# Kernel optimization log

Hardware: AMD Instinct MI355X
Metric: run time of the kernel (lower is better)

## Reference

```python
import jax, jax.numpy as jnp
import numpy as np

L = 5          # num_layer
D = 128        # emb_dim
F = 16         # raw node/edge feature dim
N = 50000      # nodes
E = 800000     # edges
BN_EPS = 1e-5


def _bn(z, g, b):
    # BatchNorm1d forward with batch statistics (training-mode math)
    m = z.mean(axis=0)
    v = z.var(axis=0)
    return (z - m) * jax.lax.rsqrt(v + BN_EPS) * g + b


def setup_inputs() -> dict:
    key = jax.random.key(0)
    ks = jax.random.split(key, 8)
    s = lambda *sh: 0.05  # weight scale
    return {
        "x": jax.random.normal(ks[0], (N, F), jnp.float32),
        "edge_index": jax.random.randint(ks[1], (2, E), 0, N, jnp.int32),
        "edge_attr": jax.random.normal(ks[2], (E, F), jnp.float32),
        "W_node": jax.random.normal(ks[3], (F, D), jnp.float32) * 0.05,
        "b_node": jnp.zeros((D,), jnp.float32),
        "We": jax.random.normal(ks[4], (L, F, D), jnp.float32) * 0.05,
        "be": jnp.zeros((L, D), jnp.float32),
        "eps_gin": jnp.zeros((L,), jnp.float32),
        "W1": jax.random.normal(ks[5], (L, D, 2 * D), jnp.float32) * 0.05,
        "b1": jnp.zeros((L, 2 * D), jnp.float32),
        "g1": jnp.ones((L, 2 * D), jnp.float32),
        "beta1": jnp.zeros((L, 2 * D), jnp.float32),
        "W2": jax.random.normal(ks[6], (L, 2 * D, D), jnp.float32) * 0.05,
        "b2": jnp.zeros((L, D), jnp.float32),
        "g_bn": jnp.ones((L, D), jnp.float32),
        "beta_bn": jnp.zeros((L, D), jnp.float32),
    }


def reference(x, edge_index, edge_attr, W_node, b_node, We, be, eps_gin,
              W1, b1, g1, beta1, W2, b2, g_bn, beta_bn):
    src, dst = edge_index[0], edge_index[1]
    n = x.shape[0]
    h = x @ W_node + b_node                       # node encoder: [N, D]
    for l in range(L):
        e = edge_attr @ We[l] + be[l]             # edge encoder: [E, D]
        msg = jax.nn.relu(h[src] + e)             # gather + message
        agg = jax.ops.segment_sum(msg, dst, num_segments=n)  # scatter-add
        z = (1.0 + eps_gin[l]) * h + agg
        z = _bn(z @ W1[l] + b1[l], g1[l], beta1[l])  # GIN MLP hidden
        z = jax.nn.relu(z)
        z = z @ W2[l] + b2[l]                     # GIN MLP out: [N, D]
        z = _bn(z, g_bn[l], beta_bn[l])           # per-layer BatchNorm
        if l < L - 1:
            z = jax.nn.relu(z)                    # dropout is identity (p=0)
        h = z + h                                 # residual
    return h                                      # JK = 'last'
```

## Files before the change

kernel.cpp:

```cpp
#include <hip/hip_runtime.h>
#include <hip/hip_bf16.h>

#define NN 50000
#define EE 800000
#define DD 128
#define FF 16
#define LL 5
#define NPART 3125

typedef __attribute__((ext_vector_type(8))) short bf16x8;
typedef __attribute__((ext_vector_type(4))) float f32x4;

__device__ __forceinline__ unsigned short f2bf(float f) {
    union { float f; unsigned int u; } v; v.f = f;
    unsigned int u = v.u;
    unsigned int r = (u + 0x7fffu + ((u >> 16) & 1u)) >> 16;
    return (unsigned short)r;
}
__device__ __forceinline__ float bf2f(unsigned short s) {
    union { unsigned int u; float f; } v; v.u = ((unsigned int)s) << 16;
    return v.f;
}
#define BFLO(u) __uint_as_float((unsigned int)(u) << 16)
#define BFHI(u) __uint_as_float((unsigned int)(u) & 0xffff0000u)

__global__ void k_node_enc(const float* __restrict__ x, const float* __restrict__ Wn,
                           const float* __restrict__ bn, float* __restrict__ h,
                           unsigned short* __restrict__ h_bf)
{
    const int t = blockIdx.x * 256 + threadIdx.x;
    const int i = t >> 7, d = t & 127;
    const float4* x4 = (const float4*)(x + (size_t)i * 16);
    float4 a0 = x4[0], a1 = x4[1], a2 = x4[2], a3 = x4[3];
    float acc = bn[d];
    acc += a0.x*Wn[0*128+d] + a0.y*Wn[1*128+d] + a0.z*Wn[2*128+d] + a0.w*Wn[3*128+d];
    acc += a1.x*Wn[4*128+d] + a1.y*Wn[5*128+d] + a1.z*Wn[6*128+d] + a1.w*Wn[7*128+d];
    acc += a2.x*Wn[8*128+d] + a2.y*Wn[9*128+d] + a2.z*Wn[10*128+d] + a2.w*Wn[11*128+d];
    acc += a3.x*Wn[12*128+d] + a3.y*Wn[13*128+d] + a3.z*Wn[14*128+d] + a3.w*Wn[15*128+d];
    h[t] = acc;
    h_bf[t] = f2bf(acc);
}

__global__ void k_count(const int* __restrict__ ei, int* __restrict__ counts)
{
    const int e = blockIdx.x * 256 + threadIdx.x;
    atomicAdd(&counts[ei[EE + e]], 1);
}

__global__ __launch_bounds__(1024) void k_scan(int* __restrict__ counts, int* __restrict__ row_ptr)
{
    __shared__ int wsum[16];
    __shared__ int carry;
    const int tid = threadIdx.x, lane = tid & 63, w = tid >> 6;
    if (tid == 0) carry = 0;
    __syncthreads();
    for (int base = 0; base < NN; base += 1024) {
        const int i = base + tid;
        const int v = (i < NN) ? counts[i] : 0;
        int x = v;
        #pragma unroll
        for (int off = 1; off < 64; off <<= 1) {
            const int t = __shfl_up(x, off);
            if (lane >= off) x += t;
        }
        if (lane == 63) wsum[w] = x;
        __syncthreads();
        int woff = 0, total = 0;
        #pragma unroll
        for (int j = 0; j < 16; ++j) { const int s = wsum[j]; total += s; if (j < w) woff += s; }
        const int ex = carry + woff + x - v;
        if (i < NN) { row_ptr[i] = ex; counts[i] = ex; }
        __syncthreads();
        if (tid == 0) carry += total;
        __syncthreads();
    }
    if (tid == 0) row_ptr[NN] = carry;
}

__global__ void k_fill(const int* __restrict__ ei, const float* __restrict__ ea,
                       int* __restrict__ cursor, int* __restrict__ src_perm,
                       unsigned short* __restrict__ ea_bf)
{
    const int e = blockIdx.x * 256 + threadIdx.x;
    const int dst = ei[EE + e];
    const int p = atomicAdd(&cursor[dst], 1);
    src_perm[p] = ei[e];
    const float4* s4 = (const float4*)(ea + (size_t)e * 16);
    const float4 a0 = s4[0], a1 = s4[1], a2 = s4[2], a3 = s4[3];
    union { bf16x8 v; unsigned short u[8]; } o0, o1;
    o0.u[0]=f2bf(a0.x); o0.u[1]=f2bf(a0.y); o0.u[2]=f2bf(a0.z); o0.u[3]=f2bf(a0.w);
    o0.u[4]=f2bf(a1.x); o0.u[5]=f2bf(a1.y); o0.u[6]=f2bf(a1.z); o0.u[7]=f2bf(a1.w);
    o1.u[0]=f2bf(a2.x); o1.u[1]=f2bf(a2.y); o1.u[2]=f2bf(a2.z); o1.u[3]=f2bf(a2.w);
    o1.u[4]=f2bf(a3.x); o1.u[5]=f2bf(a3.y); o1.u[6]=f2bf(a3.z); o1.u[7]=f2bf(a3.w);
    bf16x8* dp = (bf16x8*)(ea_bf + (size_t)p * 16);
    dp[0] = o0.v; dp[1] = o1.v;
}

__global__ void k_pack(const float* __restrict__ W1, const float* __restrict__ W2,
                       unsigned short* __restrict__ Wp1, unsigned short* __restrict__ Wp2)
{
    int t = blockIdx.x * 256 + threadIdx.x;
    const int total = LL * 32768;
    if (t < total) {
        const int l = t >> 15, r = t & 32767;
        const int j = r & 7, lane = (r >> 3) & 63, kt = (r >> 9) & 3, nt = r >> 11;
        const int k = kt * 32 + (lane >> 4) * 8 + j;
        const int n = nt * 16 + (lane & 15);
        Wp1[t] = f2bf(W1[(size_t)l * 32768 + k * 256 + n]);
    } else {
        t -= total;
        const int l = t >> 15, r = t & 32767;
        const int j = r & 7, lane = (r >> 3) & 63, kt = (r >> 9) & 7, nt = r >> 12;
        const int k = kt * 32 + (lane >> 4) * 8 + j;
        const int n = nt * 16 + (lane & 15);
        Wp2[t] = f2bf(W2[(size_t)l * 32768 + k * 128 + n]);
    }
}

__global__ __launch_bounds__(256) void k_agg(
    const unsigned short* __restrict__ h_bf, const unsigned short* __restrict__ ea_bf,
    const float* __restrict__ We_l, const float* __restrict__ be_l,
    const float* __restrict__ eps_gin, const int l,
    const int* __restrict__ row_ptr, const int* __restrict__ src_perm,
    unsigned short* __restrict__ z_bf)
{
    const int wv = threadIdx.x >> 6;
    const int v  = blockIdx.x * 4 + wv;
    const int lane = threadIdx.x & 63;
    const int c2 = lane * 2;
    float2 w[16];
    #pragma unroll
    for (int f = 0; f < 16; ++f) w[f] = *(const float2*)(We_l + f * 128 + c2);
    const float2 bed = *(const float2*)(be_l + c2);
    const float epsv = 1.0f + eps_gin[l];
    const int kbeg = __builtin_amdgcn_readfirstlane(row_ptr[v]);
    const int kend = __builtin_amdgcn_readfirstlane(row_ptr[v + 1]);
    float2 acc0 = {0.f,0.f}, acc1 = {0.f,0.f}, acc2 = {0.f,0.f}, acc3 = {0.f,0.f};

#define LOAD_GROUP(kk, S0,S1,S2,S3, E0,E1,E2,E3,E4,E5,E6,E7, H0,H1,H2,H3)  \
    { const int* sp_ = src_perm + (kk);                                     \
      S0 = __builtin_amdgcn_readfirstlane(sp_[0]);                          \
      S1 = __builtin_amdgcn_readfirstlane(sp_[1]);                          \
      S2 = __builtin_amdgcn_readfirstlane(sp_[2]);                          \
      S3 = __builtin_amdgcn_readfirstlane(sp_[3]);                          \
      const uint4* ep_ = (const uint4*)(ea_bf + (size_t)(kk) * 16);         \
      E0 = ep_[0]; E1 = ep_[1]; E2 = ep_[2]; E3 = ep_[3];                   \
      E4 = ep_[4]; E5 = ep_[5]; E6 = ep_[6]; E7 = ep_[7];                   \
      H0 = *(const unsigned int*)(h_bf + (size_t)S0 * 128 + c2);            \
      H1 = *(const unsigned int*)(h_bf + (size_t)S1 * 128 + c2);            \
      H2 = *(const unsigned int*)(h_bf + (size_t)S2 * 128 + c2);            \
      H3 = *(const unsigned int*)(h_bf + (size_t)S3 * 128 + c2); }

#define EDGE_DOT(EA, EB, HQ, OUT) do {                                      \
        float ex_ = bed.x, ey_ = bed.y, a_;                                 \
        a_ = BFLO(EA.x); ex_ += a_*w[0].x;  ey_ += a_*w[0].y;               \
        a_ = BFHI(EA.x); ex_ += a_*w[1].x;  ey_ += a_*w[1].y;               \
        a_ = BFLO(EA.y); ex_ += a_*w[2].x;  ey_ += a_*w[2].y;               \
        a_ = BFHI(EA.y); ex_ += a_*w[3].x;  ey_ += a_*w[3].y;               \
        a_ = BFLO(EA.z); ex_ += a_*w[4].x;  ey_ += a_*w[4].y;               \
        a_ = BFHI(EA.z); ex_ += a_*w[5].x;  ey_ += a_*w[5].y;               \
        a_ = BFLO(EA.w); ex_ += a_*w[6].x;  ey_ += a_*w[6].y;               \
        a_ = BFHI(EA.w); ex_ += a_*w[7].x;  ey_ += a_*w[7].y;               \
        a_ = BFLO(EB.x); ex_ += a_*w[8].x;  ey_ += a_*w[8].y;               \
        a_ = BFHI(EB.x); ex_ += a_*w[9].x;  ey_ += a_*w[9].y;               \
        a_ = BFLO(EB.y); ex_ += a_*w[10].x; ey_ += a_*w[10].y;              \
        a_ = BFHI(EB.y); ex_ += a_*w[11].x; ey_ += a_*w[11].y;              \
        a_ = BFLO(EB.z); ex_ += a_*w[12].x; ey_ += a_*w[12].y;              \
        a_ = BFHI(EB.z); ex_ += a_*w[13].x; ey_ += a_*w[13].y;              \
        a_ = BFLO(EB.w); ex_ += a_*w[14].x; ey_ += a_*w[14].y;              \
        a_ = BFHI(EB.w); ex_ += a_*w[15].x; ey_ += a_*w[15].y;              \
        const float mx_ = BFLO(HQ) + ex_, my_ = BFHI(HQ) + ey_;             \
        OUT.x += mx_ > 0.f ? mx_ : 0.f;                                     \
        OUT.y += my_ > 0.f ? my_ : 0.f;                                     \
    } while (0)

    int k = kbeg;
    int cs0, cs1, cs2, cs3;
    uint4 ce0, ce1, ce2, ce3, ce4, ce5, ce6, ce7;
    unsigned int ch0, ch1, ch2, ch3;
    if (k < kend) {
        LOAD_GROUP(k, cs0,cs1,cs2,cs3, ce0,ce1,ce2,ce3,ce4,ce5,ce6,ce7, ch0,ch1,ch2,ch3);
    }
    for (; k < kend; k += 4) {
        int ns0, ns1, ns2, ns3;
        uint4 ne0, ne1, ne2, ne3, ne4, ne5, ne6, ne7;
        unsigned int nh0, nh1, nh2, nh3;
        LOAD_GROUP(k + 4, ns0,ns1,ns2,ns3, ne0,ne1,ne2,ne3,ne4,ne5,ne6,ne7, nh0,nh1,nh2,nh3);
        EDGE_DOT(ce0, ce1, ch0, acc0);
        if (k + 1 < kend) EDGE_DOT(ce2, ce3, ch1, acc1);
        if (k + 2 < kend) EDGE_DOT(ce4, ce5, ch2, acc2);
        if (k + 3 < kend) EDGE_DOT(ce6, ce7, ch3, acc3);
        cs0=ns0; cs1=ns1; cs2=ns2; cs3=ns3;
        ce0=ne0; ce1=ne1; ce2=ne2; ce3=ne3; ce4=ne4; ce5=ne5; ce6=ne6; ce7=ne7;
        ch0=nh0; ch1=nh1; ch2=nh2; ch3=nh3;
    }
#undef EDGE_DOT
#undef LOAD_GROUP
    (void)cs0; (void)cs1; (void)cs2; (void)cs3;
    const unsigned int hv = *(const unsigned int*)(h_bf + (size_t)v * 128 + c2);
    const float zx = epsv * BFLO(hv) + ((acc0.x + acc1.x) + (acc2.x + acc3.x));
    const float zy = epsv * BFHI(hv) + ((acc0.y + acc1.y) + (acc2.y + acc3.y));
    const unsigned int zp = (unsigned int)f2bf(zx) | ((unsigned int)f2bf(zy) << 16);
    *(unsigned int*)(z_bf + (size_t)v * 128 + c2) = zp;
}

__global__ __launch_bounds__(256) void k_gemmB(
    const unsigned short* __restrict__ z_bf,
    const unsigned short* __restrict__ Wp,
    unsigned short* __restrict__ t_bf,
    float* __restrict__ ps, float* __restrict__ pq)
{
    __shared__ __align__(16) unsigned short zs[16 * 136];
    const int tid = threadIdx.x;
    const int r0 = blockIdx.x * 16;
    {
        const int row = tid & 15, c0 = (tid >> 4) * 8;
        *(bf16x8*)(&zs[row * 136 + c0]) =
            *(const bf16x8*)(z_bf + (size_t)(r0 + row) * 128 + c0);
    }
    __syncthreads();
    const int w = tid >> 6, l6 = tid & 63, m = l6 & 15, quad = l6 >> 4;
    const f32x4 z4 = {0.f, 0.f, 0.f, 0.f};
    f32x4 acc[4] = {z4, z4, z4, z4};
    const bf16x8* Wv = (const bf16x8*)Wp;
    #pragma unroll
    for (int kt = 0; kt < 4; ++kt) {
        const bf16x8 a = *(const bf16x8*)(&zs[m * 136 + kt * 32 + quad * 8]);
        #pragma unroll
        for (int f = 0; f < 4; ++f) {
            const bf16x8 b = Wv[((w * 4 + f) * 4 + kt) * 64 + l6];
            acc[f] = __builtin_amdgcn_mfma_f32_16x16x32_bf16(a, b, acc[f], 0, 0, 0);
        }
    }
    const int rowb = r0 + quad * 4;
    #pragma unroll
    for (int f = 0; f < 4; ++f) {
        const int col = w * 64 + f * 16 + m;
        float ssum = 0.f, ssq = 0.f;
        #pragma unroll
        for (int r = 0; r < 4; ++r) {
            const float val = acc[f][r];
            t_bf[(size_t)(rowb + r) * 256 + col] = f2bf(val);
            ssum += val; ssq += val * val;
        }
        ssum += __shfl_xor(ssum, 16); ssum += __shfl_xor(ssum, 32);
        ssq  += __shfl_xor(ssq , 16); ssq  += __shfl_xor(ssq , 32);
        if (quad == 0) {
            ps[(size_t)col * NPART + blockIdx.x] = ssum;
            pq[(size_t)col * NPART + blockIdx.x] = ssq;
        }
    }
}

__global__ void k_bnstat(const float* __restrict__ ps, const float* __restrict__ pq,
                         const float* __restrict__ g, const float* __restrict__ beta,
                         float* __restrict__ sc, float* __restrict__ sh)
{
    const int c = blockIdx.x;
    const int tid = threadIdx.x;
    const float* pr = ps + (size_t)c * NPART;
    const float* qr = pq + (size_t)c * NPART;
    float s = 0.f, q = 0.f;
    for (int i = tid; i < NPART; i += 256) { s += pr[i]; q += qr[i]; }
    #pragma unroll
    for (int off = 1; off < 64; off <<= 1) { s += __shfl_xor(s, off); q += __shfl_xor(q, off); }
    __shared__ float ls[4], lq[4];
    const int wv = tid >> 6;
    if ((tid & 63) == 0) { ls[wv] = s; lq[wv] = q; }
    __syncthreads();
    if (tid == 0) {
        const float S = ls[0] + ls[1] + ls[2] + ls[3];
        const float Q = lq[0] + lq[1] + lq[2] + lq[3];
        const float mean = S * (1.0f / NN);
        const float var  = Q * (1.0f / NN) - mean * mean;
        const float rs = rsqrtf(var + 1e-5f);
        const float scale = g[c] * rs;
        sc[c] = scale;
        sh[c] = beta[c] - mean * scale;
    }
}

__global__ __launch_bounds__(128) void k_gemmD(
    const unsigned short* __restrict__ t_bf,
    const float* __restrict__ sc1, const float* __restrict__ sh1,
    const unsigned short* __restrict__ Wp,
    unsigned short* __restrict__ vb,
    float* __restrict__ ps, float* __restrict__ pq)
{
    __shared__ __align__(16) unsigned short us[16 * 264];
    const int tid = threadIdx.x;
    const int r0 = blockIdx.x * 16;
    {
        const int row = tid & 15, g8 = (tid >> 4) * 8;
        #pragma unroll
        for (int cc = 0; cc < 4; ++cc) {
            const int c = cc * 64 + g8;
            union { bf16x8 v; unsigned short u[8]; } in, o;
            in.v = *(const bf16x8*)(t_bf + (size_t)(r0 + row) * 256 + c);
            const float4* scp = (const float4*)(sc1 + c);
            const float4* shp = (const float4*)(sh1 + c);
            const float4 s0 = scp[0], s1 = scp[1], b0 = shp[0], b1 = shp[1];
            float xv;
            xv = bf2f(in.u[0])*s0.x + b0.x; o.u[0] = f2bf(xv > 0.f ? xv : 0.f);
            xv = bf2f(in.u[1])*s0.y + b0.y; o.u[1] = f2bf(xv > 0.f ? xv : 0.f);
            xv = bf2f(in.u[2])*s0.z + b0.z; o.u[2] = f2bf(xv > 0.f ? xv : 0.f);
            xv = bf2f(in.u[3])*s0.w + b0.w; o.u[3] = f2bf(xv > 0.f ? xv : 0.f);
            xv = bf2f(in.u[4])*s1.x + b1.x; o.u[4] = f2bf(xv > 0.f ? xv : 0.f);
            xv = bf2f(in.u[5])*s1.y + b1.y; o.u[5] = f2bf(xv > 0.f ? xv : 0.f);
            xv = bf2f(in.u[6])*s1.z + b1.z; o.u[6] = f2bf(xv > 0.f ? xv : 0.f);
            xv = bf2f(in.u[7])*s1.w + b1.w; o.u[7] = f2bf(xv > 0.f ? xv : 0.f);
            *(bf16x8*)(&us[row * 264 + c]) = o.v;
        }
    }
    __syncthreads();
    const int w = tid >> 6, l6 = tid & 63, m = l6 & 15, quad = l6 >> 4;
    const f32x4 z4 = {0.f, 0.f, 0.f, 0.f};
    f32x4 acc[4] = {z4, z4, z4, z4};
    const bf16x8* Wv = (const bf16x8*)Wp;
    #pragma unroll
    for (int kt = 0; kt < 8; ++kt) {
        const bf16x8 a = *(const bf16x8*)(&us[m * 264 + kt * 32 + quad * 8]);
        #pragma unroll
        for (int f = 0; f < 4; ++f) {
            const bf16x8 b = Wv[((w * 4 + f) * 8 + kt) * 64 + l6];
            acc[f] = __builtin_amdgcn_mfma_f32_16x16x32_bf16(a, b, acc[f], 0, 0, 0);
        }
    }
    const int rowb = r0 + quad * 4;
    #pragma unroll
    for (int f = 0; f < 4; ++f) {
        const int col = w * 64 + f * 16 + m;
        float ssum = 0.f, ssq = 0.f;
        #pragma unroll
        for (int r = 0; r < 4; ++r) {
            const float val = acc[f][r];
            vb[(size_t)(rowb + r) * 128 + col] = f2bf(val);
            ssum += val; ssq += val * val;
        }
        ssum += __shfl_xor(ssum, 16); ssum += __shfl_xor(ssum, 32);
        ssq  += __shfl_xor(ssq , 16); ssq  += __shfl_xor(ssq , 32);
        if (quad == 0) {
            ps[(size_t)col * NPART + blockIdx.x] = ssum;
            pq[(size_t)col * NPART + blockIdx.x] = ssq;
        }
    }
}

__global__ void k_fin(const unsigned short* __restrict__ vb,
                      const float* __restrict__ sc2, const float* __restrict__ sh2,
                      float* __restrict__ h, unsigned short* __restrict__ h_bf,
                      const int do_relu)
{
    const int t = blockIdx.x * 256 + threadIdx.x;
    const int base = t * 8;
    const int c = base & 127;
    union { bf16x8 v; unsigned short u[8]; } in, ob;
    in.v = *(const bf16x8*)(vb + base);
    const float4 s0 = *(const float4*)(sc2 + c), s1 = *(const float4*)(sc2 + c + 4);
    const float4 b0 = *(const float4*)(sh2 + c), b1 = *(const float4*)(sh2 + c + 4);
    float4 h0 = *(const float4*)(h + base), h1 = *(const float4*)(h + base + 4);
    float z;
    z = bf2f(in.u[0])*s0.x + b0.x; if (do_relu) z = z > 0.f ? z : 0.f; h0.x += z;
    z = bf2f(in.u[1])*s0.y + b0.y; if (do_relu) z = z > 0.f ? z : 0.f; h0.y += z;
    z = bf2f(in.u[2])*s0.z + b0.z; if (do_relu) z = z > 0.f ? z : 0.f; h0.z += z;
    z = bf2f(in.u[3])*s0.w + b0.w; if (do_relu) z = z > 0.f ? z : 0.f; h0.w += z;
    z = bf2f(in.u[4])*s1.x + b1.x; if (do_relu) z = z > 0.f ? z : 0.f; h1.x += z;
    z = bf2f(in.u[5])*s1.y + b1.y; if (do_relu) z = z > 0.f ? z : 0.f; h1.y += z;
    z = bf2f(in.u[6])*s1.z + b1.z; if (do_relu) z = z > 0.f ? z : 0.f; h1.z += z;
    z = bf2f(in.u[7])*s1.w + b1.w; if (do_relu) z = z > 0.f ? z : 0.f; h1.w += z;
    *(float4*)(h + base) = h0;
    *(float4*)(h + base + 4) = h1;
    ob.u[0]=f2bf(h0.x); ob.u[1]=f2bf(h0.y); ob.u[2]=f2bf(h0.z); ob.u[3]=f2bf(h0.w);
    ob.u[4]=f2bf(h1.x); ob.u[5]=f2bf(h1.y); ob.u[6]=f2bf(h1.z); ob.u[7]=f2bf(h1.w);
    *(bf16x8*)(h_bf + base) = ob.v;
}

extern "C" void kernel_launch(void* const* d_in, const int* in_sizes, int n_in,
                              void* d_out, int out_size, void* d_ws, size_t ws_size,
                              hipStream_t stream)
{
    const float* x       = (const float*)d_in[0];
    const int*   ei      = (const int*)  d_in[1];
    const float* ea      = (const float*)d_in[2];
    const float* W_node  = (const float*)d_in[3];
    const float* b_node  = (const float*)d_in[4];
    const float* We      = (const float*)d_in[5];
    const float* be      = (const float*)d_in[6];
    const float* eps_gin = (const float*)d_in[7];
    const float* W1      = (const float*)d_in[8];
    const float* g1      = (const float*)d_in[10];
    const float* beta1   = (const float*)d_in[11];
    const float* W2      = (const float*)d_in[12];
    const float* g_bn    = (const float*)d_in[14];
    const float* beta_bn = (const float*)d_in[15];

    float* h = (float*)d_out;

    char* W = (char*)d_ws;
    int*   counts   = (int*)  (W + 0);
    int*   row_ptr  = (int*)  (W + 200000);
    float* sc1      = (float*)(W + 400016);
    float* sh1      = (float*)(W + 401040);
    float* sc2      = (float*)(W + 402064);
    float* sh2      = (float*)(W + 402576);
    float* ps1      = (float*)(W + 403088);
    float* pq1      = (float*)(W + 3603088);
    float* ps2      = (float*)(W + 6803088);
    float* pq2      = (float*)(W + 8403088);
    int*   src_perm = (int*)  (W + 10003088);
    unsigned short* ea_bf = (unsigned short*)(W + 13203120);
    unsigned short* Wp1   = (unsigned short*)(W + 38803376);
    unsigned short* Wp2   = (unsigned short*)(W + 39131056);
    unsigned short* z_bf  = (unsigned short*)(W + 39458736);
    unsigned short* t_bf  = (unsigned short*)(W + 52258736);
    unsigned short* h_bf  = (unsigned short*)(W + 77858736);
    unsigned short* vb    = z_bf;

    (void)hipMemsetAsync(counts, 0, 200000, stream);
    (void)hipMemsetAsync(src_perm + EE, 0, 32, stream);

    k_node_enc<<<dim3(NN * DD / 256), dim3(256), 0, stream>>>(x, W_node, b_node, h, h_bf);
    k_count<<<dim3(EE / 256), dim3(256), 0, stream>>>(ei, counts);
    k_scan<<<dim3(1), dim3(1024), 0, stream>>>(counts, row_ptr);
    k_fill<<<dim3(EE / 256), dim3(256), 0, stream>>>(ei, ea, counts, src_perm, ea_bf);
    k_pack<<<dim3(2 * LL * 32768 / 256), dim3(256), 0, stream>>>(W1, W2, Wp1, Wp2);

    for (int l = 0; l < LL; ++l) {
        k_agg<<<dim3(NN / 4), dim3(256), 0, stream>>>(
            h_bf, ea_bf, We + (size_t)l * FF * DD, be + (size_t)l * DD,
            eps_gin, l, row_ptr, src_perm, z_bf);
        k_gemmB<<<dim3(NPART), dim3(256), 0, stream>>>(
            z_bf, Wp1 + (size_t)l * 32768, t_bf, ps1, pq1);
        k_bnstat<<<dim3(256), dim3(256), 0, stream>>>(
            ps1, pq1, g1 + (size_t)l * 256, beta1 + (size_t)l * 256, sc1, sh1);
        k_gemmD<<<dim3(NPART), dim3(128), 0, stream>>>(
            t_bf, sc1, sh1, Wp2 + (size_t)l * 32768, vb, ps2, pq2);
        k_bnstat<<<dim3(128), dim3(256), 0, stream>>>(
            ps2, pq2, g_bn + (size_t)l * 128, beta_bn + (size_t)l * 128, sc2, sh2);
        k_fin<<<dim3(NN * DD / 8 / 256), dim3(256), 0, stream>>>(
            vb, sc2, sh2, h, h_bf, (l < LL - 1) ? 1 : 0);
    }
}
```

Measured before the change: 949.9 us.

## Retile GIN GEMMs to 64-row blocks and deepen index prefetch in aggregation

The two MLP GEMM kernels now process 64 rows per block, with each wave computing a 16-row strip across all output columns. This cuts the block count and raises the MFMA work done per block, with guarded tail rows and per-wave partial statistics. The aggregation kernel prefetches source indices two groups ahead and adds a scheduling barrier so gather latency overlaps compute. The tradeoffs are higher register pressure, fewer blocks to fill the GPU, and extra padding in the index buffer.

Result: slower. 1.051 ms (+10.7%).

```diff
diff --git a/kernel.cpp b/kernel.cpp
--- a/kernel.cpp
+++ b/kernel.cpp
@@ -6,7 +6,8 @@
 #define DD 128
 #define FF 16
 #define LL 5
-#define NPART 3125
+#define NB 782
+#define NPART (NB * 4)
 
 typedef __attribute__((ext_vector_type(8))) short bf16x8;
 typedef __attribute__((ext_vector_type(4))) float f32x4;
@@ -136,20 +137,6 @@
     const int kbeg = __builtin_amdgcn_readfirstlane(row_ptr[v]);
     const int kend = __builtin_amdgcn_readfirstlane(row_ptr[v + 1]);
     float2 acc0 = {0.f,0.f}, acc1 = {0.f,0.f}, acc2 = {0.f,0.f}, acc3 = {0.f,0.f};
-
-#define LOAD_GROUP(kk, S0,S1,S2,S3, E0,E1,E2,E3,E4,E5,E6,E7, H0,H1,H2,H3)  \
-    { const int* sp_ = src_perm + (kk);                                     \
-      S0 = __builtin_amdgcn_readfirstlane(sp_[0]);                          \
-      S1 = __builtin_amdgcn_readfirstlane(sp_[1]);                          \
-      S2 = __builtin_amdgcn_readfirstlane(sp_[2]);                          \
-      S3 = __builtin_amdgcn_readfirstlane(sp_[3]);                          \
-      const uint4* ep_ = (const uint4*)(ea_bf + (size_t)(kk) * 16);         \
-      E0 = ep_[0]; E1 = ep_[1]; E2 = ep_[2]; E3 = ep_[3];                   \
-      E4 = ep_[4]; E5 = ep_[5]; E6 = ep_[6]; E7 = ep_[7];                   \
-      H0 = *(const unsigned int*)(h_bf + (size_t)S0 * 128 + c2);            \
-      H1 = *(const unsigned int*)(h_bf + (size_t)S1 * 128 + c2);            \
-      H2 = *(const unsigned int*)(h_bf + (size_t)S2 * 128 + c2);            \
-      H3 = *(const unsigned int*)(h_bf + (size_t)S3 * 128 + c2); }
 
 #define EDGE_DOT(EA, EB, HQ, OUT) do {                                      \
         float ex_ = bed.x, ey_ = bed.y, a_;                                 \
@@ -174,29 +161,50 @@
         OUT.y += my_ > 0.f ? my_ : 0.f;                                     \
     } while (0)
 
-    int k = kbeg;
-    int cs0, cs1, cs2, cs3;
     uint4 ce0, ce1, ce2, ce3, ce4, ce5, ce6, ce7;
     unsigned int ch0, ch1, ch2, ch3;
+    int vs0, vs1, vs2, vs3;
+
+    int k = kbeg;
     if (k < kend) {
-        LOAD_GROUP(k, cs0,cs1,cs2,cs3, ce0,ce1,ce2,ce3,ce4,ce5,ce6,ce7, ch0,ch1,ch2,ch3);
+        const int a0 = __builtin_amdgcn_readfirstlane(src_perm[k]);
+        const int a1 = __builtin_amdgcn_readfirstlane(src_perm[k + 1]);
+        const int a2 = __builtin_amdgcn_readfirstlane(src_perm[k + 2]);
+        const int a3 = __builtin_amdgcn_readfirstlane(src_perm[k + 3]);
+        ch0 = *(const unsigned int*)(h_bf + (size_t)a0 * 128 + c2);
+        ch1 = *(const unsigned int*)(h_bf + (size_t)a1 * 128 + c2);
+        ch2 = *(const unsigned int*)(h_bf + (size_t)a2 * 128 + c2);
+        ch3 = *(const unsigned int*)(h_bf + (size_t)a3 * 128 + c2);
+        const uint4* ep = (const uint4*)(ea_bf + (size_t)k * 16);
+        ce0 = ep[0]; ce1 = ep[1]; ce2 = ep[2]; ce3 = ep[3];
+        ce4 = ep[4]; ce5 = ep[5]; ce6 = ep[6]; ce7 = ep[7];
+        vs0 = src_perm[k + 4]; vs1 = src_perm[k + 5];
+        vs2 = src_perm[k + 6]; vs3 = src_perm[k + 7];
     }
     for (; k < kend; k += 4) {
-        int ns0, ns1, ns2, ns3;
-        uint4 ne0, ne1, ne2, ne3, ne4, ne5, ne6, ne7;
-        unsigned int nh0, nh1, nh2, nh3;
-        LOAD_GROUP(k + 4, ns0,ns1,ns2,ns3, ne0,ne1,ne2,ne3,ne4,ne5,ne6,ne7, nh0,nh1,nh2,nh3);
+        const int fs0 = src_perm[k + 8],  fs1 = src_perm[k + 9];
+        const int fs2 = src_perm[k + 10], fs3 = src_perm[k + 11];
+        const int b0 = __builtin_amdgcn_readfirstlane(vs0);
+        const int b1 = __builtin_amdgcn_readfirstlane(vs1);
+        const int b2 = __builtin_amdgcn_readfirstlane(vs2);
+        const int b3 = __builtin_amdgcn_readfirstlane(vs3);
+        const unsigned int nh0 = *(const unsigned int*)(h_bf + (size_t)b0 * 128 + c2);
+        const unsigned int nh1 = *(const unsigned int*)(h_bf + (size_t)b1 * 128 + c2);
+        const unsigned int nh2 = *(const unsigned int*)(h_bf + (size_t)b2 * 128 + c2);
+        const unsigned int nh3 = *(const unsigned int*)(h_bf + (size_t)b3 * 128 + c2);
+        const uint4* np_ = (const uint4*)(ea_bf + (size_t)(k + 4) * 16);
+        const uint4 ne0 = np_[0], ne1 = np_[1], ne2 = np_[2], ne3 = np_[3];
+        const uint4 ne4 = np_[4], ne5 = np_[5], ne6 = np_[6], ne7 = np_[7];
+        __builtin_amdgcn_sched_barrier(0);
         EDGE_DOT(ce0, ce1, ch0, acc0);
         if (k + 1 < kend) EDGE_DOT(ce2, ce3, ch1, acc1);
         if (k + 2 < kend) EDGE_DOT(ce4, ce5, ch2, acc2);
         if (k + 3 < kend) EDGE_DOT(ce6, ce7, ch3, acc3);
-        cs0=ns0; cs1=ns1; cs2=ns2; cs3=ns3;
         ce0=ne0; ce1=ne1; ce2=ne2; ce3=ne3; ce4=ne4; ce5=ne5; ce6=ne6; ce7=ne7;
         ch0=nh0; ch1=nh1; ch2=nh2; ch3=nh3;
+        vs0=fs0; vs1=fs1; vs2=fs2; vs3=fs3;
     }
 #undef EDGE_DOT
-#undef LOAD_GROUP
-    (void)cs0; (void)cs1; (void)cs2; (void)cs3;
     const unsigned int hv = *(const unsigned int*)(h_bf + (size_t)v * 128 + c2);
     const float zx = epsv * BFLO(hv) + ((acc0.x + acc1.x) + (acc2.x + acc3.x));
     const float zy = epsv * BFHI(hv) + ((acc0.y + acc1.y) + (acc2.y + acc3.y));
@@ -210,44 +218,49 @@
     unsigned short* __restrict__ t_bf,
     float* __restrict__ ps, float* __restrict__ pq)
 {
-    __shared__ __align__(16) unsigned short zs[16 * 136];
+    __shared__ __align__(16) unsigned short zs[64 * 136];
     const int tid = threadIdx.x;
-    const int r0 = blockIdx.x * 16;
+    const int r0 = blockIdx.x * 64;
     {
-        const int row = tid & 15, c0 = (tid >> 4) * 8;
-        *(bf16x8*)(&zs[row * 136 + c0]) =
-            *(const bf16x8*)(z_bf + (size_t)(r0 + row) * 128 + c0);
+        const int rb = tid >> 4, c0 = (tid & 15) * 8;
+        const bf16x8 zero = {0,0,0,0,0,0,0,0};
+        #pragma unroll
+        for (int r = 0; r < 4; ++r) {
+            const int row = r * 16 + rb, g = r0 + row;
+            *(bf16x8*)(&zs[row * 136 + c0]) =
+                (g < NN) ? *(const bf16x8*)(z_bf + (size_t)g * 128 + c0) : zero;
+        }
     }
     __syncthreads();
     const int w = tid >> 6, l6 = tid & 63, m = l6 & 15, quad = l6 >> 4;
     const f32x4 z4 = {0.f, 0.f, 0.f, 0.f};
-    f32x4 acc[4] = {z4, z4, z4, z4};
+    f32x4 acc[16] = {z4,z4,z4,z4,z4,z4,z4,z4,z4,z4,z4,z4,z4,z4,z4,z4};
     const bf16x8* Wv = (const bf16x8*)Wp;
     #pragma unroll
     for (int kt = 0; kt < 4; ++kt) {
-        const bf16x8 a = *(const bf16x8*)(&zs[m * 136 + kt * 32 + quad * 8]);
-        #pragma unroll
-        for (int f = 0; f < 4; ++f) {
-            const bf16x8 b = Wv[((w * 4 + f) * 4 + kt) * 64 + l6];
-            acc[f] = __builtin_amdgcn_mfma_f32_16x16x32_bf16(a, b, acc[f], 0, 0, 0);
-        }
-    }
-    const int rowb = r0 + quad * 4;
-    #pragma unroll
-    for (int f = 0; f < 4; ++f) {
-        const int col = w * 64 + f * 16 + m;
+        const bf16x8 a = *(const bf16x8*)(&zs[(w * 16 + m) * 136 + kt * 32 + quad * 8]);
+        #pragma unroll
+        for (int ct = 0; ct < 16; ++ct) {
+            const bf16x8 b = Wv[(ct * 4 + kt) * 64 + l6];
+            acc[ct] = __builtin_amdgcn_mfma_f32_16x16x32_bf16(a, b, acc[ct], 0, 0, 0);
+        }
+    }
+    const int rowb = r0 + w * 16 + quad * 4;
+    #pragma unroll
+    for (int ct = 0; ct < 16; ++ct) {
+        const int col = ct * 16 + m;
         float ssum = 0.f, ssq = 0.f;
         #pragma unroll
         for (int r = 0; r < 4; ++r) {
-            const float val = acc[f][r];
-            t_bf[(size_t)(rowb + r) * 256 + col] = f2bf(val);
+            const float val = acc[ct][r];
+            if (rowb + r < NN) t_bf[(size_t)(rowb + r) * 256 + col] = f2bf(val);
             ssum += val; ssq += val * val;
         }
         ssum += __shfl_xor(ssum, 16); ssum += __shfl_xor(ssum, 32);
         ssq  += __shfl_xor(ssq , 16); ssq  += __shfl_xor(ssq , 32);
         if (quad == 0) {
-            ps[(size_t)col * NPART + blockIdx.x] = ssum;
-            pq[(size_t)col * NPART + blockIdx.x] = ssq;
+            ps[(size_t)col * NPART + blockIdx.x * 4 + w] = ssum;
+            pq[(size_t)col * NPART + blockIdx.x * 4 + w] = ssq;
         }
     }
 }
@@ -280,68 +293,72 @@
     }
 }
 
-__global__ __launch_bounds__(128) void k_gemmD(
+__global__ __launch_bounds__(256) void k_gemmD(
     const unsigned short* __restrict__ t_bf,
     const float* __restrict__ sc1, const float* __restrict__ sh1,
     const unsigned short* __restrict__ Wp,
     unsigned short* __restrict__ vb,
     float* __restrict__ ps, float* __restrict__ pq)
 {
-    __shared__ __align__(16) unsigned short us[16 * 264];
+    __shared__ __align__(16) unsigned short us[64 * 264];
     const int tid = threadIdx.x;
-    const int r0 = blockIdx.x * 16;
+    const int r0 = blockIdx.x * 64;
     {
-        const int row = tid & 15, g8 = (tid >> 4) * 8;
-        #pragma unroll
-        for (int cc = 0; cc < 4; ++cc) {
-            const int c = cc * 64 + g8;
+        const int rb = tid >> 5, c0 = (tid & 31) * 8;
+        const float4 s0 = *(const float4*)(sc1 + c0), s1 = *(const float4*)(sc1 + c0 + 4);
+        const float4 b0 = *(const float4*)(sh1 + c0), b1 = *(const float4*)(sh1 + c0 + 4);
+        const bf16x8 zero = {0,0,0,0,0,0,0,0};
+        #pragma unroll
+        for (int rr = 0; rr < 8; ++rr) {
+            const int row = rr * 8 + rb, g = r0 + row;
             union { bf16x8 v; unsigned short u[8]; } in, o;
-            in.v = *(const bf16x8*)(t_bf + (size_t)(r0 + row) * 256 + c);
-            const float4* scp = (const float4*)(sc1 + c);
-            const float4* shp = (const float4*)(sh1 + c);
-            const float4 s0 = scp[0], s1 = scp[1], b0 = shp[0], b1 = shp[1];
-            float xv;
-            xv = bf2f(in.u[0])*s0.x + b0.x; o.u[0] = f2bf(xv > 0.f ? xv : 0.f);
-            xv = bf2f(in.u[1])*s0.y + b0.y; o.u[1] = f2bf(xv > 0.f ? xv : 0.f);
-            xv = bf2f(in.u[2])*s0.z + b0.z; o.u[2] = f2bf(xv > 0.f ? xv : 0.f);
-            xv = bf2f(in.u[3])*s0.w + b0.w; o.u[3] = f2bf(xv > 0.f ? xv : 0.f);
-            xv = bf2f(in.u[4])*s1.x + b1.x; o.u[4] = f2bf(xv > 0.f ? xv : 0.f);
-            xv = bf2f(in.u[5])*s1.y + b1.y; o.u[5] = f2bf(xv > 0.f ? xv : 0.f);
-            xv = bf2f(in.u[6])*s1.z + b1.z; o.u[6] = f2bf(xv > 0.f ? xv : 0.f);
-            xv = bf2f(in.u[7])*s1.w + b1.w; o.u[7] = f2bf(xv > 0.f ? xv : 0.f);
-            *(bf16x8*)(&us[row * 264 + c]) = o.v;
+            if (g < NN) {
+                in.v = *(const bf16x8*)(t_bf + (size_t)g * 256 + c0);
+                float xv;
+                xv = bf2f(in.u[0])*s0.x + b0.x; o.u[0] = f2bf(xv > 0.f ? xv : 0.f);
+                xv = bf2f(in.u[1])*s0.y + b0.y; o.u[1] = f2bf(xv > 0.f ? xv : 0.f);
+                xv = bf2f(in.u[2])*s0.z + b0.z; o.u[2] = f2bf(xv > 0.f ? xv : 0.f);
+                xv = bf2f(in.u[3])*s0.w + b0.w; o.u[3] = f2bf(xv > 0.f ? xv : 0.f);
+                xv = bf2f(in.u[4])*s1.x + b1.x; o.u[4] = f2bf(xv > 0.f ? xv : 0.f);
+                xv = bf2f(in.u[5])*s1.y + b1.y; o.u[5] = f2bf(xv > 0.f ? xv : 0.f);
+                xv = bf2f(in.u[6])*s1.z + b1.z; o.u[6] = f2bf(xv > 0.f ? xv : 0.f);
+                xv = bf2f(in.u[7])*s1.w + b1.w; o.u[7] = f2bf(xv > 0.f ? xv : 0.f);
+            } else {
+                o.v = zero;
+            }
+            *(bf16x8*)(&us[row * 264 + c0]) = o.v;
         }
     }
     __syncthreads();
     const int w = tid >> 6, l6 = tid & 63, m = l6 & 15, quad = l6 >> 4;
     const f32x4 z4 = {0.f, 0.f, 0.f, 0.f};
-    f32x4 acc[4] = {z4, z4, z4, z4};
+    f32x4 acc[8] = {z4,z4,z4,z4,z4,z4,z4,z4};
     const bf16x8* Wv = (const bf16x8*)Wp;
     #pragma unroll
     for (int kt = 0; kt < 8; ++kt) {
-        const bf16x8 a = *(const bf16x8*)(&us[m * 264 + kt * 32 + quad * 8]);
-        #pragma unroll
-        for (int f = 0; f < 4; ++f) {
-            const bf16x8 b = Wv[((w * 4 + f) * 8 + kt) * 64 + l6];
-            acc[f] = __builtin_amdgcn_mfma_f32_16x16x32_bf16(a, b, acc[f], 0, 0, 0);
-        }
-    }
-    const int rowb = r0 + quad * 4;
-    #pragma unroll
-    for (int f = 0; f < 4; ++f) {
-        const int col = w * 64 + f * 16 + m;
+        const bf16x8 a = *(const bf16x8*)(&us[(w * 16 + m) * 264 + kt * 32 + quad * 8]);
+        #pragma unroll
+        for (int ct = 0; ct < 8; ++ct) {
+            const bf16x8 b = Wv[(ct * 8 + kt) * 64 + l6];
+            acc[ct] = __builtin_amdgcn_mfma_f32_16x16x32_bf16(a, b, acc[ct], 0, 0, 0);
+        }
+    }
+    const int rowb = r0 + w * 16 + quad * 4;
+    #pragma unroll
+    for (int ct = 0; ct < 8; ++ct) {
+        const int col = ct * 16 + m;
         float ssum = 0.f, ssq = 0.f;
         #pragma unroll
         for (int r = 0; r < 4; ++r) {
-            const float val = acc[f][r];
-            vb[(size_t)(rowb + r) * 128 + col] = f2bf(val);
+            const float val = acc[ct][r];
+            if (rowb + r < NN) vb[(size_t)(rowb + r) * 128 + col] = f2bf(val);
             ssum += val; ssq += val * val;
         }
         ssum += __shfl_xor(ssum, 16); ssum += __shfl_xor(ssum, 32);
         ssq  += __shfl_xor(ssq , 16); ssq  += __shfl_xor(ssq , 32);
         if (quad == 0) {
-            ps[(size_t)col * NPART + blockIdx.x] = ssum;
-            pq[(size_t)col * NPART + blockIdx.x] = ssq;
+            ps[(size_t)col * NPART + blockIdx.x * 4 + w] = ssum;
+            pq[(size_t)col * NPART + blockIdx.x * 4 + w] = ssq;
         }
     }
 }
@@ -399,25 +416,25 @@
     char* W = (char*)d_ws;
     int*   counts   = (int*)  (W + 0);
     int*   row_ptr  = (int*)  (W + 200000);
-    float* sc1      = (float*)(W + 400016);
-    float* sh1      = (float*)(W + 401040);
-    float* sc2      = (float*)(W + 402064);
-    float* sh2      = (float*)(W + 402576);
-    float* ps1      = (float*)(W + 403088);
-    float* pq1      = (float*)(W + 3603088);
-    float* ps2      = (float*)(W + 6803088);
-    float* pq2      = (float*)(W + 8403088);
-    int*   src_perm = (int*)  (W + 10003088);
-    unsigned short* ea_bf = (unsigned short*)(W + 13203120);
-    unsigned short* Wp1   = (unsigned short*)(W + 38803376);
-    unsigned short* Wp2   = (unsigned short*)(W + 39131056);
-    unsigned short* z_bf  = (unsigned short*)(W + 39458736);
-    unsigned short* t_bf  = (unsigned short*)(W + 52258736);
-    unsigned short* h_bf  = (unsigned short*)(W + 77858736);
+    float* sc1      = (float*)(W + 400064);
+    float* sh1      = (float*)(W + 401088);
+    float* sc2      = (float*)(W + 402112);
+    float* sh2      = (float*)(W + 402624);
+    float* ps1      = (float*)(W + 403136);
+    float* pq1      = (float*)(W + 3606208);
+    float* ps2      = (float*)(W + 6809280);
+    float* pq2      = (float*)(W + 8410816);
+    int*   src_perm = (int*)  (W + 10012352);
+    unsigned short* ea_bf = (unsigned short*)(W + 13212416);
+    unsigned short* Wp1   = (unsigned short*)(W + 38812928);
+    unsigned short* Wp2   = (unsigned short*)(W + 39140608);
+    unsigned short* z_bf  = (unsigned short*)(W + 39468288);
+    unsigned short* t_bf  = (unsigned short*)(W + 52268288);
+    unsigned short* h_bf  = (unsigned short*)(W + 77868288);
     unsigned short* vb    = z_bf;
 
     (void)hipMemsetAsync(counts, 0, 200000, stream);
-    (void)hipMemsetAsync(src_perm + EE, 0, 32, stream);
+    (void)hipMemsetAsync(src_perm + EE, 0, 64, stream);
 
     k_node_enc<<<dim3(NN * DD / 256), dim3(256), 0, stream>>>(x, W_node, b_node, h, h_bf);
     k_count<<<dim3(EE / 256), dim3(256), 0, stream>>>(ei, counts);
@@ -429,11 +446,11 @@
         k_agg<<<dim3(NN / 4), dim3(256), 0, stream>>>(
             h_bf, ea_bf, We + (size_t)l * FF * DD, be + (size_t)l * DD,
             eps_gin, l, row_ptr, src_perm, z_bf);
-        k_gemmB<<<dim3(NPART), dim3(256), 0, stream>>>(
+        k_gemmB<<<dim3(NB), dim3(256), 0, stream>>>(
             z_bf, Wp1 + (size_t)l * 32768, t_bf, ps1, pq1);
         k_bnstat<<<dim3(256), dim3(256), 0, stream>>>(
             ps1, pq1, g1 + (size_t)l * 256, beta1 + (size_t)l * 256, sc1, sh1);
-        k_gemmD<<<dim3(NPART), dim3(128), 0, stream>>>(
+        k_gemmD<<<dim3(NB), dim3(256), 0, stream>>>(
             t_bf, sc1, sh1, Wp2 + (size_t)l * 32768, vb, ps2, pq2);
         k_bnstat<<<dim3(128), dim3(256), 0, stream>>>(
             ps2, pq2, g_bn + (size_t)l * 128, beta_bn + (size_t)l * 128, sc2, sh2);
```
